# Optimization experiments

Measured on AMD Instinct MI355X. Metric: run time of the kernel, lower is better.

## Reference

```python
import jax, jax.numpy as jnp
import numpy as np

EPS = 1e-5

def _segment_mean(src_feat, edge_index, num_targets):
    # src_feat: [Ns, D]; edge_index: [2, E] = [source_idx, target_idx]
    msgs = src_feat[edge_index[0]]                                   # [E, D] gather
    agg = jax.ops.segment_sum(msgs, edge_index[1], num_segments=num_targets)
    deg = jax.ops.segment_sum(jnp.ones((edge_index.shape[1],), src_feat.dtype),
                              edge_index[1], num_segments=num_targets)
    return agg / jnp.clip(deg, 1.0)[:, None]

def _layernorm(x, gamma, beta):
    mu = jnp.mean(x, axis=-1, keepdims=True)
    var = jnp.mean(jnp.square(x - mu), axis=-1, keepdims=True)
    return (x - mu) * jax.lax.rsqrt(var + EPS) * gamma + beta

def setup_inputs() -> dict:
    key = jax.random.key(0)
    ks = jax.random.split(key, 8)
    NU, NI, E, D = 50000, 50000, 300000, 256
    s = 1.0 / np.sqrt(D)
    return {
        "user_features": jax.random.normal(ks[0], (NU, D), jnp.float32),
        "item_features": jax.random.normal(ks[1], (NI, D), jnp.float32),
        "user_item_edge_index": jax.random.randint(ks[2], (2, E), 0, NI),
        "item_user_edge_index": jax.random.randint(ks[3], (2, E), 0, NU),
        "Wu": jax.random.uniform(ks[4], (D, D), jnp.float32, -s, s),
        "bu": jax.random.uniform(ks[5], (D,), jnp.float32, -s, s),
        "Wi": jax.random.uniform(ks[6], (D, D), jnp.float32, -s, s),
        "bi": jax.random.uniform(ks[7], (D,), jnp.float32, -s, s),
        "gamma": jnp.ones((D,), jnp.float32),
        "beta": jnp.zeros((D,), jnp.float32),
    }

def reference(user_features, item_features, user_item_edge_index, item_user_edge_index,
              Wu, bu, Wi, bi, gamma, beta):
    num_items = item_features.shape[0]
    num_users = user_features.shape[0]
    # messages into items come from users; into users come from items
    item_messages = _segment_mean(user_features, user_item_edge_index, num_items)
    user_messages = _segment_mean(item_features, item_user_edge_index, num_users)
    u_new = (user_features + user_messages) @ Wu + bu
    i_new = (item_features + item_messages) @ Wi + bi
    u_new = _layernorm(jax.nn.relu(u_new), gamma, beta)
    i_new = _layernorm(jax.nn.relu(i_new), gamma, beta)
    return (u_new, i_new)
```

## Files before the change

kernel.cpp:

```cpp
#include <hip/hip_runtime.h>
#include <hip/hip_bf16.h>

#define D 256
#define BM 64
#define BK 64
#define LDK 72

typedef __attribute__((ext_vector_type(8))) __bf16 bf16x8;
typedef __attribute__((ext_vector_type(4))) float f32x4;

__device__ __forceinline__ float bf2f(unsigned short u) {
    union { unsigned int i; float f; } c; c.i = ((unsigned int)u) << 16; return c.f;
}
__device__ __forceinline__ unsigned short f2bf(float f) {
    __hip_bfloat16 h = __float2bfloat16(f);
    return *reinterpret_cast<unsigned short*>(&h);
}


__global__ void k_cvt_all(const float* __restrict__ uf, const float* __restrict__ itf,
                          const float* __restrict__ Wu, const float* __restrict__ Wi,
                          unsigned short* __restrict__ feat_bf,
                          unsigned short* __restrict__ Wt_u, unsigned short* __restrict__ Wt_i,
                          size_t nfU, size_t nfTot, int nbF) {
    int b = blockIdx.x;
    if (b < nbF) {
        size_t base = ((size_t)b * 256 + threadIdx.x) * 8;
        if (base < nfTot) {
            const float* s = (base < nfU) ? (uf + base) : (itf + (base - nfU));
            float4 f0 = *(const float4*)s;
            float4 f1 = *(const float4*)(s + 4);
            ushort4 o0, o1;
            o0.x = f2bf(f0.x); o0.y = f2bf(f0.y); o0.z = f2bf(f0.z); o0.w = f2bf(f0.w);
            o1.x = f2bf(f1.x); o1.y = f2bf(f1.y); o1.z = f2bf(f1.z); o1.w = f2bf(f1.w);
            ((ushort4*)(feat_bf + base))[0] = o0;
            ((ushort4*)(feat_bf + base))[1] = o1;
        }
    } else {
        int b2 = b - nbF;
        const float* W = (b2 < 256) ? Wu : Wi;
        unsigned short* Wt = (b2 < 256) ? Wt_u : Wt_i;
        int k = b2 & 255;
        int c = threadIdx.x;
        Wt[(size_t)c * 256 + k] = f2bf(W[(size_t)k * 256 + c]);
    }
}

__global__ void k_hist2(const int* __restrict__ iu_e, int Eiu,
                        const int* __restrict__ ui_e, int Eui,
                        int* __restrict__ deg, int NU) {
    int e = blockIdx.x * blockDim.x + threadIdx.x;
    if (e < Eiu) {
        atomicAdd(&deg[iu_e[Eiu + e]], 1);
    } else if (e < Eiu + Eui) {
        int e2 = e - Eiu;
        atomicAdd(&deg[NU + ui_e[Eui + e2]], 1);
    }
}

__global__ void k_scan_block(const int* __restrict__ deg, int N,
                             int* __restrict__ rs, int* __restrict__ bsums) {
    __shared__ int s[1024];
    int base = blockIdx.x * 1024;
    int t = threadIdx.x;
    int v = (base + t < N) ? deg[base + t] : 0;
    s[t] = v;
    __syncthreads();
    for (int off = 1; off < 1024; off <<= 1) {
        int add = (t >= off) ? s[t - off] : 0;
        __syncthreads();
        s[t] += add;
        __syncthreads();
    }
    if (base + t < N) rs[base + t + 1] = s[t];
    if (t == 1023) bsums[blockIdx.x] = s[1023];
}

__global__ void k_scan_sums(int* __restrict__ bsums, int nb) {
    __shared__ int s[1024];
    int t = threadIdx.x;
    int v = (t < nb) ? bsums[t] : 0;
    s[t] = v;
    __syncthreads();
    for (int off = 1; off < 1024; off <<= 1) {
        int add = (t >= off) ? s[t - off] : 0;
        __syncthreads();
        s[t] += add;
        __syncthreads();
    }
    if (t < nb) bsums[t] = s[t] - v;
}

__global__ void k_finalize(int N, int* __restrict__ rs, int* __restrict__ cur,
                           const int* __restrict__ bsums) {
    int i = blockIdx.x * blockDim.x + threadIdx.x;
    if (i < N) {
        int v = rs[i + 1] + bsums[i >> 10];
        rs[i + 1] = v;
        cur[i + 1] = v;
    }
    if (i == 0) { rs[0] = 0; cur[0] = 0; }
}

__global__ void k_fill2(const int* __restrict__ iu_e, int Eiu,
                        const int* __restrict__ ui_e, int Eui,
                        int* __restrict__ cur, int NU,
                        int* __restrict__ csr) {
    int e = blockIdx.x * blockDim.x + threadIdx.x;
    if (e < Eiu) {
        int d = iu_e[Eiu + e];
        int p = atomicAdd(&cur[d], 1);
        csr[p] = iu_e[e];
    } else if (e < Eiu + Eui) {
        int e2 = e - Eiu;
        int d = ui_e[Eui + e2];
        int p = atomicAdd(&cur[NU + d], 1);
        csr[p] = ui_e[e2];
    }
}

__global__ void k_msg2(const unsigned short* __restrict__ uf_bf,
                       const unsigned short* __restrict__ if_bf,
                       const int* __restrict__ rs, const int* __restrict__ csr,
                       unsigned short* __restrict__ x_u, unsigned short* __restrict__ x_i,
                       int NU, int NI) {
    int wv = (blockIdx.x * blockDim.x + threadIdx.x) >> 6;
    int lane = threadIdx.x & 63;
    if (wv >= NU + NI) return;
    const unsigned short* src; const unsigned short* tgt; unsigned short* xo; int w;
    if (wv < NU) { src = if_bf; tgt = uf_bf; xo = x_u; w = wv; }
    else         { src = uf_bf; tgt = if_bf; xo = x_i; w = wv - NU; }

    int s0 = rs[wv], s1 = rs[wv + 1];
    float ax0=0,ay0=0,az0=0,aw0=0, ax1=0,ay1=0,az1=0,aw1=0;
    float ax2=0,ay2=0,az2=0,aw2=0, ax3=0,ay3=0,az3=0,aw3=0;
    int i = s0;
    for (; i + 4 <= s1; i += 4) {
        int e0 = csr[i], e1 = csr[i+1], e2 = csr[i+2], e3 = csr[i+3];
        ushort4 r0 = ((const ushort4*)(src + (size_t)e0 * D))[lane];
        ushort4 r1 = ((const ushort4*)(src + (size_t)e1 * D))[lane];
        ushort4 r2 = ((const ushort4*)(src + (size_t)e2 * D))[lane];
        ushort4 r3 = ((const ushort4*)(src + (size_t)e3 * D))[lane];
        ax0 += bf2f(r0.x); ay0 += bf2f(r0.y); az0 += bf2f(r0.z); aw0 += bf2f(r0.w);
        ax1 += bf2f(r1.x); ay1 += bf2f(r1.y); az1 += bf2f(r1.z); aw1 += bf2f(r1.w);
        ax2 += bf2f(r2.x); ay2 += bf2f(r2.y); az2 += bf2f(r2.z); aw2 += bf2f(r2.w);
        ax3 += bf2f(r3.x); ay3 += bf2f(r3.y); az3 += bf2f(r3.z); aw3 += bf2f(r3.w);
    }
    if (i + 2 <= s1) {
        int e0 = csr[i], e1 = csr[i+1];
        ushort4 r0 = ((const ushort4*)(src + (size_t)e0 * D))[lane];
        ushort4 r1 = ((const ushort4*)(src + (size_t)e1 * D))[lane];
        ax0 += bf2f(r0.x); ay0 += bf2f(r0.y); az0 += bf2f(r0.z); aw0 += bf2f(r0.w);
        ax1 += bf2f(r1.x); ay1 += bf2f(r1.y); az1 += bf2f(r1.z); aw1 += bf2f(r1.w);
        i += 2;
    }
    if (i < s1) {
        int e0 = csr[i];
        ushort4 r0 = ((const ushort4*)(src + (size_t)e0 * D))[lane];
        ax2 += bf2f(r0.x); ay2 += bf2f(r0.y); az2 += bf2f(r0.z); aw2 += bf2f(r0.w);
    }
    float sx = (ax0 + ax1) + (ax2 + ax3);
    float sy = (ay0 + ay1) + (ay2 + ay3);
    float sz = (az0 + az1) + (az2 + az3);
    float sw = (aw0 + aw1) + (aw2 + aw3);
    int cnt = s1 - s0;
    float inv = 1.0f / (float)(cnt > 0 ? cnt : 1);
    ushort4 tv = ((const ushort4*)(tgt + (size_t)w * D))[lane];
    ushort4 o;
    o.x = f2bf(bf2f(tv.x) + sx * inv);
    o.y = f2bf(bf2f(tv.y) + sy * inv);
    o.z = f2bf(bf2f(tv.z) + sz * inv);
    o.w = f2bf(bf2f(tv.w) + sw * inv);
    ((ushort4*)(xo + (size_t)w * D))[lane] = o;
}

__launch_bounds__(256)
__global__ void k_gemm2(const unsigned short* __restrict__ x_u,
                        const unsigned short* __restrict__ x_i,
                        const unsigned short* __restrict__ Wt_u,
                        const unsigned short* __restrict__ Wt_i,
                        const float* __restrict__ bu, const float* __restrict__ bi,
                        const float* __restrict__ gamma, const float* __restrict__ beta,
                        int NU, int NI, int nbU, float* __restrict__ out) {
    __shared__ __hip_bfloat16 As[BM][LDK];
    __shared__ __hip_bfloat16 Bs[D][LDK];
    __shared__ float red_s[BM][4];
    __shared__ float red_q[BM][4];

    int b = blockIdx.x;
    bool isU = b < nbU;
    const unsigned short* X  = isU ? x_u : x_i;
    const unsigned short* Wt = isU ? Wt_u : Wt_i;
    const float* bias        = isU ? bu : bi;
    float* Y                 = isU ? out : out + (size_t)NU * D;
    int N                    = isU ? NU : NI;
    int row0 = (isU ? b : b - nbU) * BM;

    int t = threadIdx.x;
    int lane = t & 63;
    int w = t >> 6;
    int l15 = lane & 15;
    int l4 = lane >> 4;

    f32x4 acc[4][4];
    f32x4 zero = {0.f, 0.f, 0.f, 0.f};
    #pragma unroll
    for (int fr = 0; fr < 4; fr++)
        #pragma unroll
        for (int fc = 0; fc < 4; fc++)
            acc[fr][fc] = zero;

    for (int k0 = 0; k0 < D; k0 += BK) {
        {
            int i = t >> 2;
            int kq = (t & 3) * 16;
            int r = row0 + i;
            uint4 b0 = {0,0,0,0}, b1 = {0,0,0,0};
            if (r < N) {
                const uint4* p = (const uint4*)&X[(size_t)r * D + k0 + kq];
                b0 = p[0]; b1 = p[1];
            }
            *(uint4*)&As[i][kq]     = b0;
            *(uint4*)&As[i][kq + 8] = b1;
        }
        #pragma unroll
        for (int pass = 0; pass < 4; pass++) {
            int c = pass * 64 + (t >> 2);
            int kq = (t & 3) * 16;
            const uint4* p = (const uint4*)&Wt[(size_t)c * D + k0 + kq];
            uint4 b0 = p[0], b1 = p[1];
            *(uint4*)&Bs[c][kq]     = b0;
            *(uint4*)&Bs[c][kq + 8] = b1;
        }
        __syncthreads();

        #pragma unroll
        for (int ks = 0; ks < 2; ks++) {
            bf16x8 af[4], bg[4];
            #pragma unroll
            for (int fr = 0; fr < 4; fr++)
                af[fr] = *(const bf16x8*)&As[fr * 16 + l15][ks * 32 + l4 * 8];
            #pragma unroll
            for (int fc = 0; fc < 4; fc++)
                bg[fc] = *(const bf16x8*)&Bs[w * 64 + fc * 16 + l15][ks * 32 + l4 * 8];
            #pragma unroll
            for (int fr = 0; fr < 4; fr++)
                #pragma unroll
                for (int fc = 0; fc < 4; fc++)
                    acc[fr][fc] = __builtin_amdgcn_mfma_f32_16x16x32_bf16(
                        af[fr], bg[fc], acc[fr][fc], 0, 0, 0);
        }
        __syncthreads();
    }

    float bias_c[4], gam_c[4], bet_c[4];
    #pragma unroll
    for (int fc = 0; fc < 4; fc++) {
        int col = w * 64 + fc * 16 + l15;
        bias_c[fc] = bias[col];
        gam_c[fc]  = gamma[col];
        bet_c[fc]  = beta[col];
    }

    #pragma unroll
    for (int fr = 0; fr < 4; fr++) {
        #pragma unroll
        for (int r = 0; r < 4; r++) {
            int row = fr * 16 + l4 * 4 + r;
            float s = 0.f, q = 0.f;
            #pragma unroll
            for (int fc = 0; fc < 4; fc++) {
                float v = acc[fr][fc][r] + bias_c[fc];
                v = fmaxf(v, 0.f);
                acc[fr][fc][r] = v;
                s += v;
                q += v * v;
            }
            #pragma unroll
            for (int m = 1; m < 16; m <<= 1) {
                s += __shfl_xor(s, m);
                q += __shfl_xor(q, m);
            }
            if (l15 == 0) { red_s[row][w] = s; red_q[row][w] = q; }
        }
    }
    __syncthreads();

    #pragma unroll
    for (int fr = 0; fr < 4; fr++) {
        #pragma unroll
        for (int r = 0; r < 4; r++) {
            int row = fr * 16 + l4 * 4 + r;
            int grow = row0 + row;
            if (grow >= N) continue;
            float s = red_s[row][0] + red_s[row][1] + red_s[row][2] + red_s[row][3];
            float q = red_q[row][0] + red_q[row][1] + red_q[row][2] + red_q[row][3];
            float mu  = s * (1.0f / 256.0f);
            float var = q * (1.0f / 256.0f) - mu * mu;
            float rstd = rsqrtf(var + 1e-5f);
            #pragma unroll
            for (int fc = 0; fc < 4; fc++) {
                int col = w * 64 + fc * 16 + l15;
                Y[(size_t)grow * D + col] = (acc[fr][fc][r] - mu) * rstd * gam_c[fc] + bet_c[fc];
            }
        }
    }
}


__global__ void k_hist(const int* __restrict__ dst, int E, int* __restrict__ deg) {
    int e = blockIdx.x * blockDim.x + threadIdx.x;
    if (e < E) atomicAdd(&deg[dst[e]], 1);
}

__global__ void k_finalize_rs(int N, int* __restrict__ rs, const int* __restrict__ bsums) {
    int i = blockIdx.x * blockDim.x + threadIdx.x;
    if (i < N) rs[i + 1] += bsums[i >> 10];
    if (i == 0) rs[0] = 0;
}

__global__ void k_fill(const int* __restrict__ src, const int* __restrict__ dst, int E,
                       const int* __restrict__ rs, int* __restrict__ cursor,
                       int* __restrict__ csr) {
    int e = blockIdx.x * blockDim.x + threadIdx.x;
    if (e < E) {
        int d = dst[e];
        int p = atomicAdd(&cursor[d], 1);
        csr[rs[d] + p] = src[e];
    }
}

__global__ void k_msg_x(const float* __restrict__ srcf, const float* __restrict__ tgtf,
                        const int* __restrict__ rs, const int* __restrict__ csr,
                        int N, float* __restrict__ xout) {
    int wave = (blockIdx.x * blockDim.x + threadIdx.x) >> 6;
    int lane = threadIdx.x & 63;
    if (wave >= N) return;
    int s0 = rs[wave], s1 = rs[wave + 1];
    float4 acc = make_float4(0.f, 0.f, 0.f, 0.f);
    for (int i = s0; i < s1; i++) {
        int s = csr[i];
        float4 f = *(const float4*)&srcf[(size_t)s * D + lane * 4];
        acc.x += f.x; acc.y += f.y; acc.z += f.z; acc.w += f.w;
    }
    int cnt = s1 - s0;
    float inv = 1.0f / (float)(cnt > 0 ? cnt : 1);
    float4 t = *(const float4*)&tgtf[(size_t)wave * D + lane * 4];
    float4 x;
    x.x = t.x + acc.x * inv;
    x.y = t.y + acc.y * inv;
    x.z = t.z + acc.z * inv;
    x.w = t.w + acc.w * inv;
    *(float4*)&xout[(size_t)wave * D + lane * 4] = x;
}

__global__ void k_wcvt(const float* __restrict__ W0, const float* __restrict__ W1,
                       __hip_bfloat16* __restrict__ Wt0, __hip_bfloat16* __restrict__ Wt1) {
    int b = blockIdx.x;
    const float* W = (b < 256) ? W0 : W1;
    __hip_bfloat16* Wt = (b < 256) ? Wt0 : Wt1;
    int k = b & 255;
    int c = threadIdx.x;
    Wt[(size_t)c * 256 + k] = __float2bfloat16(W[(size_t)k * 256 + c]);
}

__launch_bounds__(256)
__global__ void k_gemm_mfma_ln(const float* __restrict__ X,
                               const __hip_bfloat16* __restrict__ Wt,
                               const float* __restrict__ bias,
                               const float* __restrict__ gamma,
                               const float* __restrict__ beta,
                               int N, float* __restrict__ Y) {
    __shared__ __hip_bfloat16 As[BM][LDK];
    __shared__ __hip_bfloat16 Bs[D][LDK];
    __shared__ float red_s[BM][4];
    __shared__ float red_q[BM][4];

    int t = threadIdx.x;
    int lane = t & 63;
    int w = t >> 6;
    int l15 = lane & 15;
    int l4 = lane >> 4;
    int row0 = blockIdx.x * BM;

    f32x4 acc[4][4];
    f32x4 zero = {0.f, 0.f, 0.f, 0.f};
    #pragma unroll
    for (int fr = 0; fr < 4; fr++)
        #pragma unroll
        for (int fc = 0; fc < 4; fc++)
            acc[fr][fc] = zero;

    for (int k0 = 0; k0 < D; k0 += BK) {
        {
            int i = t >> 2;
            int kq = (t & 3) * 16;
            int r = row0 + i;
            float4 f[4];
            if (r < N) {
                const float4* p = (const float4*)&X[(size_t)r * D + k0 + kq];
                f[0] = p[0]; f[1] = p[1]; f[2] = p[2]; f[3] = p[3];
            } else {
                float4 z4 = make_float4(0.f, 0.f, 0.f, 0.f);
                f[0] = z4; f[1] = z4; f[2] = z4; f[3] = z4;
            }
            __hip_bfloat16 vb[16];
            #pragma unroll
            for (int q = 0; q < 4; q++) {
                vb[q * 4 + 0] = __float2bfloat16(f[q].x);
                vb[q * 4 + 1] = __float2bfloat16(f[q].y);
                vb[q * 4 + 2] = __float2bfloat16(f[q].z);
                vb[q * 4 + 3] = __float2bfloat16(f[q].w);
            }
            *(uint4*)&As[i][kq]     = *(uint4*)&vb[0];
            *(uint4*)&As[i][kq + 8] = *(uint4*)&vb[8];
        }
        #pragma unroll
        for (int pass = 0; pass < 4; pass++) {
            int c = pass * 64 + (t >> 2);
            int kq = (t & 3) * 16;
            const uint4* p = (const uint4*)&Wt[(size_t)c * D + k0 + kq];
            uint4 b0 = p[0], b1 = p[1];
            *(uint4*)&Bs[c][kq]     = b0;
            *(uint4*)&Bs[c][kq + 8] = b1;
        }
        __syncthreads();

        #pragma unroll
        for (int ks = 0; ks < 2; ks++) {
            bf16x8 af[4], bg[4];
            #pragma unroll
            for (int fr = 0; fr < 4; fr++)
                af[fr] = *(const bf16x8*)&As[fr * 16 + l15][ks * 32 + l4 * 8];
            #pragma unroll
            for (int fc = 0; fc < 4; fc++)
                bg[fc] = *(const bf16x8*)&Bs[w * 64 + fc * 16 + l15][ks * 32 + l4 * 8];
            #pragma unroll
            for (int fr = 0; fr < 4; fr++)
                #pragma unroll
                for (int fc = 0; fc < 4; fc++)
                    acc[fr][fc] = __builtin_amdgcn_mfma_f32_16x16x32_bf16(
                        af[fr], bg[fc], acc[fr][fc], 0, 0, 0);
        }
        __syncthreads();
    }

    float bias_c[4], gam_c[4], bet_c[4];
    #pragma unroll
    for (int fc = 0; fc < 4; fc++) {
        int col = w * 64 + fc * 16 + l15;
        bias_c[fc] = bias[col];
        gam_c[fc]  = gamma[col];
        bet_c[fc]  = beta[col];
    }

    #pragma unroll
    for (int fr = 0; fr < 4; fr++) {
        #pragma unroll
        for (int r = 0; r < 4; r++) {
            int row = fr * 16 + l4 * 4 + r;
            float s = 0.f, q = 0.f;
            #pragma unroll
            for (int fc = 0; fc < 4; fc++) {
                float v = acc[fr][fc][r] + bias_c[fc];
                v = fmaxf(v, 0.f);
                acc[fr][fc][r] = v;
                s += v;
                q += v * v;
            }
            #pragma unroll
            for (int m = 1; m < 16; m <<= 1) {
                s += __shfl_xor(s, m);
                q += __shfl_xor(q, m);
            }
            if (l15 == 0) { red_s[row][w] = s; red_q[row][w] = q; }
        }
    }
    __syncthreads();

    #pragma unroll
    for (int fr = 0; fr < 4; fr++) {
        #pragma unroll
        for (int r = 0; r < 4; r++) {
            int row = fr * 16 + l4 * 4 + r;
            int grow = row0 + row;
            if (grow >= N) continue;
            float s = red_s[row][0] + red_s[row][1] + red_s[row][2] + red_s[row][3];
            float q = red_q[row][0] + red_q[row][1] + red_q[row][2] + red_q[row][3];
            float mu  = s * (1.0f / 256.0f);
            float var = q * (1.0f / 256.0f) - mu * mu;
            float rstd = rsqrtf(var + 1e-5f);
            #pragma unroll
            for (int fc = 0; fc < 4; fc++) {
                int col = w * 64 + fc * 16 + l15;
                Y[(size_t)grow * D + col] = (acc[fr][fc][r] - mu) * rstd * gam_c[fc] + bet_c[fc];
            }
        }
    }
}


extern "C" void kernel_launch(void* const* d_in, const int* in_sizes, int n_in,
                              void* d_out, int out_size, void* d_ws, size_t ws_size,
                              hipStream_t stream) {
    const float* uf    = (const float*)d_in[0];
    const float* itf   = (const float*)d_in[1];
    const int*   ui_e  = (const int*)d_in[2];
    const int*   iu_e  = (const int*)d_in[3];
    const float* Wu    = (const float*)d_in[4];
    const float* bu    = (const float*)d_in[5];
    const float* Wi    = (const float*)d_in[6];
    const float* bi    = (const float*)d_in[7];
    const float* gamma = (const float*)d_in[8];
    const float* beta  = (const float*)d_in[9];

    int NU  = in_sizes[0] / D;
    int NI  = in_sizes[1] / D;
    int Eui = in_sizes[2] / 2;
    int Eiu = in_sizes[3] / 2;
    int Nmax = NU > NI ? NU : NI;
    int Ntot = NU + NI;
    int Etot = Eiu + Eui;

    float* out   = (float*)d_out;
    size_t nfU = (size_t)NU * D;
    size_t nfI = (size_t)NI * D;
    size_t nfTot = nfU + nfI;

    unsigned short* uf_bf = (unsigned short*)d_ws;
    unsigned short* if_bf = uf_bf + nfU;
    unsigned short* x_u   = if_bf + nfI;
    unsigned short* x_i   = x_u + nfU;
    unsigned short* Wt_u2 = x_i + nfI;
    unsigned short* Wt_i2 = Wt_u2 + 65536;
    int* deg2  = (int*)(Wt_i2 + 65536);
    int* rs2   = deg2 + Ntot;
    int* cur2  = rs2 + Ntot + 1;
    int* bsums = cur2 + Ntot + 1;
    int* csr2  = bsums + 1024;
    size_t needed = (size_t)((char*)(csr2 + Etot) - (char*)d_ws);

    if (ws_size >= needed) {
        int nbF = (int)((nfTot + 2047) / 2048);
        k_cvt_all<<<nbF + 512, 256, 0, stream>>>(uf, itf, Wu, Wi, uf_bf, Wt_u2, Wt_i2,
                                                 nfU, nfTot, nbF);
        hipMemsetAsync(deg2, 0, (size_t)Ntot * sizeof(int), stream);
        k_hist2<<<(Etot + 255) / 256, 256, 0, stream>>>(iu_e, Eiu, ui_e, Eui, deg2, NU);
        int nb = (Ntot + 1023) / 1024;
        k_scan_block<<<nb, 1024, 0, stream>>>(deg2, Ntot, rs2, bsums);
        k_scan_sums<<<1, 1024, 0, stream>>>(bsums, nb);
        k_finalize<<<(Ntot + 255) / 256, 256, 0, stream>>>(Ntot, rs2, cur2, bsums);
        k_fill2<<<(Etot + 255) / 256, 256, 0, stream>>>(iu_e, Eiu, ui_e, Eui, cur2, NU, csr2);
        k_msg2<<<(Ntot + 3) / 4, 256, 0, stream>>>(uf_bf, if_bf, rs2, csr2, x_u, x_i, NU, NI);
        int nbU = (NU + BM - 1) / BM;
        int nbI = (NI + BM - 1) / BM;
        k_gemm2<<<nbU + nbI, 256, 0, stream>>>(x_u, x_i, Wt_u2, Wt_i2, bu, bi, gamma, beta,
                                               NU, NI, nbU, out);
        return;
    }

    float* u_out = out;
    float* i_out = out + nfU;
    __hip_bfloat16* Wt_u = (__hip_bfloat16*)d_ws;
    __hip_bfloat16* Wt_i = Wt_u + 256 * 256;
    int* deg    = (int*)(Wt_i + 256 * 256);
    int* rs     = deg + Nmax;
    int* bs     = rs + Nmax + 1;
    int* cursor = bs + 1024;
    int* csr    = cursor + Nmax;

    k_wcvt<<<512, 256, 0, stream>>>(Wu, Wi, Wt_u, Wt_i);

    auto run_side = [&](const float* srcf, const float* tgtf, const int* edges, int E,
                        int N, const __hip_bfloat16* Wt, const float* bias, float* y) {
        const int* esrc = edges;
        const int* edst = edges + E;
        hipMemsetAsync(deg, 0, (size_t)N * sizeof(int), stream);
        hipMemsetAsync(cursor, 0, (size_t)N * sizeof(int), stream);
        k_hist<<<(E + 255) / 256, 256, 0, stream>>>(edst, E, deg);
        int nb = (N + 1023) / 1024;
        k_scan_block<<<nb, 1024, 0, stream>>>(deg, N, rs, bs);
        k_scan_sums<<<1, 1024, 0, stream>>>(bs, nb);
        k_finalize_rs<<<(N + 255) / 256, 256, 0, stream>>>(N, rs, bs);
        k_fill<<<(E + 255) / 256, 256, 0, stream>>>(esrc, edst, E, rs, cursor, csr);
        k_msg_x<<<(N + 3) / 4, 256, 0, stream>>>(srcf, tgtf, rs, csr, N, y);
        k_gemm_mfma_ln<<<(N + BM - 1) / BM, 256, 0, stream>>>(y, Wt, bias, gamma, beta, N, y);
    };

    run_side(itf, uf, iu_e, Eiu, NU, Wt_u, bu, u_out);
    run_side(uf, itf, ui_e, Eui, NI, Wt_i, bi, i_out);
}
```

Baseline: 220.2 us.

## Prefetch GEMM tiles into registers, use half-wave gathers, fold degree memset into convert kernel

The GEMM now uses a K-tile of 32 and loads the next A and B tiles into registers while MFMAs run on the current shared-memory tile, overlapping global loads with compute. The message kernel assigns one node per half-wave with 16-byte loads, so each wave handles two nodes. Zeroing the degree array moves into the convert kernel, replacing a separate memset. In exchange the GEMM does twice as many syncs per K, and its register pressure rises.

```diff
diff --git a/kernel.cpp b/kernel.cpp
--- a/kernel.cpp
+++ b/kernel.cpp
@@ -3,7 +3,8 @@
 
 #define D 256
 #define BM 64
-#define BK 64
+#define BK2 32
+#define LDK2 40
 #define LDK 72
 
 typedef __attribute__((ext_vector_type(8))) __bf16 bf16x8;
@@ -11,10 +12,19 @@
 
 __device__ __forceinline__ float bf2f(unsigned short u) {
     union { unsigned int i; float f; } c; c.i = ((unsigned int)u) << 16; return c.f;
+}
+__device__ __forceinline__ float bf2f_lo(unsigned int u) {
+    union { unsigned int i; float f; } c; c.i = u << 16; return c.f;
+}
+__device__ __forceinline__ float bf2f_hi(unsigned int u) {
+    union { unsigned int i; float f; } c; c.i = u & 0xffff0000u; return c.f;
 }
 __device__ __forceinline__ unsigned short f2bf(float f) {
     __hip_bfloat16 h = __float2bfloat16(f);
     return *reinterpret_cast<unsigned short*>(&h);
+}
+__device__ __forceinline__ unsigned int pack2(float lo, float hi) {
+    return (unsigned int)f2bf(lo) | ((unsigned int)f2bf(hi) << 16);
 }
 
 
@@ -22,6 +32,7 @@
                           const float* __restrict__ Wu, const float* __restrict__ Wi,
                           unsigned short* __restrict__ feat_bf,
                           unsigned short* __restrict__ Wt_u, unsigned short* __restrict__ Wt_i,
+                          int* __restrict__ deg, int Ntot,
                           size_t nfU, size_t nfTot, int nbF) {
     int b = blockIdx.x;
     if (b < nbF) {
@@ -36,13 +47,21 @@
             ((ushort4*)(feat_bf + base))[0] = o0;
             ((ushort4*)(feat_bf + base))[1] = o1;
         }
-    } else {
+    } else if (b < nbF + 512) {
         int b2 = b - nbF;
         const float* W = (b2 < 256) ? Wu : Wi;
         unsigned short* Wt = (b2 < 256) ? Wt_u : Wt_i;
         int k = b2 & 255;
         int c = threadIdx.x;
         Wt[(size_t)c * 256 + k] = f2bf(W[(size_t)k * 256 + c]);
+    } else {
+        int zb = b - nbF - 512;
+        size_t base = ((size_t)zb * 256 + threadIdx.x) * 4;
+        if (base + 4 <= (size_t)Ntot) {
+            *(int4*)(deg + base) = make_int4(0, 0, 0, 0);
+        } else if (base < (size_t)Ntot) {
+            for (size_t j = base; j < (size_t)Ntot; ++j) deg[j] = 0;
+        }
     }
 }
 
@@ -124,54 +143,58 @@
                        const int* __restrict__ rs, const int* __restrict__ csr,
                        unsigned short* __restrict__ x_u, unsigned short* __restrict__ x_i,
                        int NU, int NI) {
-    int wv = (blockIdx.x * blockDim.x + threadIdx.x) >> 6;
+    int pair = (blockIdx.x * blockDim.x + threadIdx.x) >> 6;
     int lane = threadIdx.x & 63;
-    if (wv >= NU + NI) return;
+    int half = lane >> 5;
+    int hl   = lane & 31;
+    int Ntot = NU + NI;
+    int wv = pair * 2 + half;
+    if (wv >= Ntot) return;
+
     const unsigned short* src; const unsigned short* tgt; unsigned short* xo; int w;
     if (wv < NU) { src = if_bf; tgt = uf_bf; xo = x_u; w = wv; }
     else         { src = uf_bf; tgt = if_bf; xo = x_i; w = wv - NU; }
 
     int s0 = rs[wv], s1 = rs[wv + 1];
-    float ax0=0,ay0=0,az0=0,aw0=0, ax1=0,ay1=0,az1=0,aw1=0;
-    float ax2=0,ay2=0,az2=0,aw2=0, ax3=0,ay3=0,az3=0,aw3=0;
+    float a0[8] = {}, a1[8] = {}, a2[8] = {}, a3[8] = {};
+
     int i = s0;
     for (; i + 4 <= s1; i += 4) {
-        int e0 = csr[i], e1 = csr[i+1], e2 = csr[i+2], e3 = csr[i+3];
-        ushort4 r0 = ((const ushort4*)(src + (size_t)e0 * D))[lane];
-        ushort4 r1 = ((const ushort4*)(src + (size_t)e1 * D))[lane];
-        ushort4 r2 = ((const ushort4*)(src + (size_t)e2 * D))[lane];
-        ushort4 r3 = ((const ushort4*)(src + (size_t)e3 * D))[lane];
-        ax0 += bf2f(r0.x); ay0 += bf2f(r0.y); az0 += bf2f(r0.z); aw0 += bf2f(r0.w);
-        ax1 += bf2f(r1.x); ay1 += bf2f(r1.y); az1 += bf2f(r1.z); aw1 += bf2f(r1.w);
-        ax2 += bf2f(r2.x); ay2 += bf2f(r2.y); az2 += bf2f(r2.z); aw2 += bf2f(r2.w);
-        ax3 += bf2f(r3.x); ay3 += bf2f(r3.y); az3 += bf2f(r3.z); aw3 += bf2f(r3.w);
-    }
-    if (i + 2 <= s1) {
-        int e0 = csr[i], e1 = csr[i+1];
-        ushort4 r0 = ((const ushort4*)(src + (size_t)e0 * D))[lane];
-        ushort4 r1 = ((const ushort4*)(src + (size_t)e1 * D))[lane];
-        ax0 += bf2f(r0.x); ay0 += bf2f(r0.y); az0 += bf2f(r0.z); aw0 += bf2f(r0.w);
-        ax1 += bf2f(r1.x); ay1 += bf2f(r1.y); az1 += bf2f(r1.z); aw1 += bf2f(r1.w);
-        i += 2;
-    }
-    if (i < s1) {
+        int e0 = csr[i], e1 = csr[i + 1], e2 = csr[i + 2], e3 = csr[i + 3];
+        uint4 r0 = ((const uint4*)(src + (size_t)e0 * D))[hl];
+        uint4 r1 = ((const uint4*)(src + (size_t)e1 * D))[hl];
+        uint4 r2 = ((const uint4*)(src + (size_t)e2 * D))[hl];
+        uint4 r3 = ((const uint4*)(src + (size_t)e3 * D))[hl];
+        a0[0] += bf2f_lo(r0.x); a0[1] += bf2f_hi(r0.x); a0[2] += bf2f_lo(r0.y); a0[3] += bf2f_hi(r0.y);
+        a0[4] += bf2f_lo(r0.z); a0[5] += bf2f_hi(r0.z); a0[6] += bf2f_lo(r0.w); a0[7] += bf2f_hi(r0.w);
+        a1[0] += bf2f_lo(r1.x); a1[1] += bf2f_hi(r1.x); a1[2] += bf2f_lo(r1.y); a1[3] += bf2f_hi(r1.y);
+        a1[4] += bf2f_lo(r1.z); a1[5] += bf2f_hi(r1.z); a1[6] += bf2f_lo(r1.w); a1[7] += bf2f_hi(r1.w);
+        a2[0] += bf2f_lo(r2.x); a2[1] += bf2f_hi(r2.x); a2[2] += bf2f_lo(r2.y); a2[3] += bf2f_hi(r2.y);
+        a2[4] += bf2f_lo(r2.z); a2[5] += bf2f_hi(r2.z); a2[6] += bf2f_lo(r2.w); a2[7] += bf2f_hi(r2.w);
+        a3[0] += bf2f_lo(r3.x); a3[1] += bf2f_hi(r3.x); a3[2] += bf2f_lo(r3.y); a3[3] += bf2f_hi(r3.y);
+        a3[4] += bf2f_lo(r3.z); a3[5] += bf2f_hi(r3.z); a3[6] += bf2f_lo(r3.w); a3[7] += bf2f_hi(r3.w);
+    }
+    for (; i < s1; ++i) {
         int e0 = csr[i];
-        ushort4 r0 = ((const ushort4*)(src + (size_t)e0 * D))[lane];
-        ax2 += bf2f(r0.x); ay2 += bf2f(r0.y); az2 += bf2f(r0.z); aw2 += bf2f(r0.w);
-    }
-    float sx = (ax0 + ax1) + (ax2 + ax3);
-    float sy = (ay0 + ay1) + (ay2 + ay3);
-    float sz = (az0 + az1) + (az2 + az3);
-    float sw = (aw0 + aw1) + (aw2 + aw3);
+        uint4 r0 = ((const uint4*)(src + (size_t)e0 * D))[hl];
+        a0[0] += bf2f_lo(r0.x); a0[1] += bf2f_hi(r0.x); a0[2] += bf2f_lo(r0.y); a0[3] += bf2f_hi(r0.y);
+        a0[4] += bf2f_lo(r0.z); a0[5] += bf2f_hi(r0.z); a0[6] += bf2f_lo(r0.w); a0[7] += bf2f_hi(r0.w);
+    }
+
     int cnt = s1 - s0;
     float inv = 1.0f / (float)(cnt > 0 ? cnt : 1);
-    ushort4 tv = ((const ushort4*)(tgt + (size_t)w * D))[lane];
-    ushort4 o;
-    o.x = f2bf(bf2f(tv.x) + sx * inv);
-    o.y = f2bf(bf2f(tv.y) + sy * inv);
-    o.z = f2bf(bf2f(tv.z) + sz * inv);
-    o.w = f2bf(bf2f(tv.w) + sw * inv);
-    ((ushort4*)(xo + (size_t)w * D))[lane] = o;
+    uint4 tv = ((const uint4*)(tgt + (size_t)w * D))[hl];
+    float x0 = bf2f_lo(tv.x) + (a0[0] + a1[0] + a2[0] + a3[0]) * inv;
+    float x1 = bf2f_hi(tv.x) + (a0[1] + a1[1] + a2[1] + a3[1]) * inv;
+    float x2 = bf2f_lo(tv.y) + (a0[2] + a1[2] + a2[2] + a3[2]) * inv;
+    float x3 = bf2f_hi(tv.y) + (a0[3] + a1[3] + a2[3] + a3[3]) * inv;
+    float x4 = bf2f_lo(tv.z) + (a0[4] + a1[4] + a2[4] + a3[4]) * inv;
+    float x5 = bf2f_hi(tv.z) + (a0[5] + a1[5] + a2[5] + a3[5]) * inv;
+    float x6 = bf2f_lo(tv.w) + (a0[6] + a1[6] + a2[6] + a3[6]) * inv;
+    float x7 = bf2f_hi(tv.w) + (a0[7] + a1[7] + a2[7] + a3[7]) * inv;
+    uint4 o;
+    o.x = pack2(x0, x1); o.y = pack2(x2, x3); o.z = pack2(x4, x5); o.w = pack2(x6, x7);
+    ((uint4*)(xo + (size_t)w * D))[hl] = o;
 }
 
 __launch_bounds__(256)
@@ -182,8 +205,8 @@
                         const float* __restrict__ bu, const float* __restrict__ bi,
                         const float* __restrict__ gamma, const float* __restrict__ beta,
                         int NU, int NI, int nbU, float* __restrict__ out) {
-    __shared__ __hip_bfloat16 As[BM][LDK];
-    __shared__ __hip_bfloat16 Bs[D][LDK];
+    __shared__ __hip_bfloat16 As[BM][LDK2];
+    __shared__ __hip_bfloat16 Bs[D][LDK2];
     __shared__ float red_s[BM][4];
     __shared__ float red_q[BM][4];
 
@@ -202,6 +225,16 @@
     int l15 = lane & 15;
     int l4 = lane >> 4;
 
+    int ar = row0 + (t >> 2);
+    int ak = (t & 3) * 8;
+    const uint4* Ag = (const uint4*)&X[(size_t)ar * D + ak];
+    const uint4* Bg = (const uint4*)&Wt[(size_t)t * D];
+
+    uint4 uz = {0, 0, 0, 0};
+    bool aok = (ar < N);
+    uint4 aR = aok ? Ag[0] : uz;
+    uint4 bR0 = Bg[0], bR1 = Bg[1], bR2 = Bg[2], bR3 = Bg[3];
+
     f32x4 acc[4][4];
     f32x4 zero = {0.f, 0.f, 0.f, 0.f};
     #pragma unroll
@@ -210,46 +243,31 @@
         for (int fc = 0; fc < 4; fc++)
             acc[fr][fc] = zero;
 
-    for (int k0 = 0; k0 < D; k0 += BK) {
-        {
-            int i = t >> 2;
-            int kq = (t & 3) * 16;
-            int r = row0 + i;
-            uint4 b0 = {0,0,0,0}, b1 = {0,0,0,0};
-            if (r < N) {
-                const uint4* p = (const uint4*)&X[(size_t)r * D + k0 + kq];
-                b0 = p[0]; b1 = p[1];
-            }
-            *(uint4*)&As[i][kq]     = b0;
-            *(uint4*)&As[i][kq + 8] = b1;
-        }
-        #pragma unroll
-        for (int pass = 0; pass < 4; pass++) {
-            int c = pass * 64 + (t >> 2);
-            int kq = (t & 3) * 16;
-            const uint4* p = (const uint4*)&Wt[(size_t)c * D + k0 + kq];
-            uint4 b0 = p[0], b1 = p[1];
-            *(uint4*)&Bs[c][kq]     = b0;
-            *(uint4*)&Bs[c][kq + 8] = b1;
-        }
-        __syncthreads();
-
-        #pragma unroll
-        for (int ks = 0; ks < 2; ks++) {
-            bf16x8 af[4], bg[4];
-            #pragma unroll
-            for (int fr = 0; fr < 4; fr++)
-                af[fr] = *(const bf16x8*)&As[fr * 16 + l15][ks * 32 + l4 * 8];
+    for (int k0 = 0; k0 < D; k0 += BK2) {
+        *(uint4*)&As[t >> 2][ak] = aR;
+        *(uint4*)&Bs[t][0]  = bR0;
+        *(uint4*)&Bs[t][8]  = bR1;
+        *(uint4*)&Bs[t][16] = bR2;
+        *(uint4*)&Bs[t][24] = bR3;
+        __syncthreads();
+        if (k0 + BK2 < D) {
+            int kn = (k0 + BK2) >> 3;
+            aR  = aok ? Ag[kn] : uz;
+            bR0 = Bg[kn]; bR1 = Bg[kn + 1]; bR2 = Bg[kn + 2]; bR3 = Bg[kn + 3];
+        }
+        bf16x8 af[4], bg4[4];
+        #pragma unroll
+        for (int fr = 0; fr < 4; fr++)
+            af[fr] = *(const bf16x8*)&As[fr * 16 + l15][l4 * 8];
+        #pragma unroll
+        for (int fc = 0; fc < 4; fc++)
+            bg4[fc] = *(const bf16x8*)&Bs[w * 64 + fc * 16 + l15][l4 * 8];
+        #pragma unroll
+        for (int fr = 0; fr < 4; fr++)
             #pragma unroll
             for (int fc = 0; fc < 4; fc++)
-                bg[fc] = *(const bf16x8*)&Bs[w * 64 + fc * 16 + l15][ks * 32 + l4 * 8];
-            #pragma unroll
-            for (int fr = 0; fr < 4; fr++)
-                #pragma unroll
-                for (int fc = 0; fc < 4; fc++)
-                    acc[fr][fc] = __builtin_amdgcn_mfma_f32_16x16x32_bf16(
-                        af[fr], bg[fc], acc[fr][fc], 0, 0, 0);
-        }
+                acc[fr][fc] = __builtin_amdgcn_mfma_f32_16x16x32_bf16(
+                    af[fr], bg4[fc], acc[fr][fc], 0, 0, 0);
         __syncthreads();
     }
 
@@ -391,7 +409,7 @@
         for (int fc = 0; fc < 4; fc++)
             acc[fr][fc] = zero;
 
-    for (int k0 = 0; k0 < D; k0 += BK) {
+    for (int k0 = 0; k0 < D; k0 += 64) {
         {
             int i = t >> 2;
             int kq = (t & 3) * 16;
@@ -542,16 +560,17 @@
 
     if (ws_size >= needed) {
         int nbF = (int)((nfTot + 2047) / 2048);
-        k_cvt_all<<<nbF + 512, 256, 0, stream>>>(uf, itf, Wu, Wi, uf_bf, Wt_u2, Wt_i2,
-                                                 nfU, nfTot, nbF);
-        hipMemsetAsync(deg2, 0, (size_t)Ntot * sizeof(int), stream);
+        int nbZ = (Ntot + 1023) / 1024;
+        k_cvt_all<<<nbF + 512 + nbZ, 256, 0, stream>>>(uf, itf, Wu, Wi, uf_bf, Wt_u2, Wt_i2,
+                                                       deg2, Ntot, nfU, nfTot, nbF);
         k_hist2<<<(Etot + 255) / 256, 256, 0, stream>>>(iu_e, Eiu, ui_e, Eui, deg2, NU);
         int nb = (Ntot + 1023) / 1024;
         k_scan_block<<<nb, 1024, 0, stream>>>(deg2, Ntot, rs2, bsums);
         k_scan_sums<<<1, 1024, 0, stream>>>(bsums, nb);
         k_finalize<<<(Ntot + 255) / 256, 256, 0, stream>>>(Ntot, rs2, cur2, bsums);
         k_fill2<<<(Etot + 255) / 256, 256, 0, stream>>>(iu_e, Eiu, ui_e, Eui, cur2, NU, csr2);
-        k_msg2<<<(Ntot + 3) / 4, 256, 0, stream>>>(uf_bf, if_bf, rs2, csr2, x_u, x_i, NU, NI);
+        int pairs = (Ntot + 1) / 2;
+        k_msg2<<<(pairs + 3) / 4, 256, 0, stream>>>(uf_bf, if_bf, rs2, csr2, x_u, x_i, NU, NI);
         int nbU = (NU + BM - 1) / BM;
         int nbI = (NI + BM - 1) / BM;
         k_gemm2<<<nbU + nbI, 256, 0, stream>>>(x_u, x_i, Wt_u2, Wt_i2, bu, bi, gamma, beta,
```

Result: no change. 219.2 us (-0.4%).
